# Performance work log

Measured on AMD Instinct MI355X. Metric: run time of the kernel, lower is better.

The kernel has to match this reference:

```python
import jax, jax.numpy as jnp
import numpy as np


def setup_inputs() -> dict:
    key = jax.random.key(0)
    k1, k2, k3, k4 = jax.random.split(key, 4)
    N, E, F, H = 100000, 1600000, 128, 128
    x = jax.random.normal(k1, (N, F), dtype=jnp.float32)
    edge_index = jax.random.randint(k2, (2, E), 0, N, dtype=jnp.int64)
    W1 = jax.random.normal(k3, (F, H), dtype=jnp.float32) * (1.0 / np.sqrt(F))
    b1 = jnp.zeros((H,), dtype=jnp.float32)
    W2 = jax.random.normal(k4, (H, H), dtype=jnp.float32) * (1.0 / np.sqrt(H))
    b2 = jnp.zeros((H,), dtype=jnp.float32)
    return {"x": x, "edge_index": edge_index, "W1": W1, "b1": b1, "W2": W2, "b2": b2}


def reference(x, edge_index, W1, b1, W2, b2):
    # Two-layer cached GCN: norm is computed once (cached) and reused by both layers.
    N = x.shape[0]
    loops = jnp.arange(N, dtype=edge_index.dtype)
    src = jnp.concatenate([edge_index[0], loops])  # add self-loops
    dst = jnp.concatenate([edge_index[1], loops])
    # symmetric GCN normalization: deg^-1/2[src] * deg^-1/2[dst]
    deg = jax.ops.segment_sum(jnp.ones_like(dst, dtype=x.dtype), dst, num_segments=N)
    dinv = jnp.where(deg > 0, jax.lax.rsqrt(deg), 0.0)
    norm = dinv[src] * dinv[dst]  # [E+N]

    def conv(h, W, b):
        h = h @ W  # dense transform before sparse aggregate (cheaper: out_dim small)
        msg = norm[:, None] * h[src]  # gather + scale
        return jax.ops.segment_sum(msg, dst, num_segments=N) + b

    h = jax.nn.relu(conv(x, W1, b1))
    # dropout is identity in eval mode (deterministic reference)
    return conv(h, W2, b2)
```

## Files before the change

### kernel.cpp

```cpp
#include <hip/hip_runtime.h>


#define BKT_SHIFT 7
#define BKT_NODES 128
#define CH 4096
#define MAXBKT 1024

typedef _Float16 half4v __attribute__((ext_vector_type(4)));
typedef _Float16 half8v __attribute__((ext_vector_type(8)));
typedef float float4v __attribute__((ext_vector_type(4)));

__global__ __launch_bounds__(256) void k_prep(const float* __restrict__ W1,
                                              const float* __restrict__ W2,
                                              _Float16* __restrict__ wt1,
                                              _Float16* __restrict__ wt2,
                                              int* __restrict__ bcnt,
                                              int* __restrict__ dcnt, int nbkt) {
    int i = blockIdx.x * 256 + threadIdx.x;
    if (i < 16384) {
        int k = i >> 7, c = i & 127;
        wt1[c * 128 + k] = (_Float16)W1[i];
    } else {
        int j = i - 16384;
        int k = j >> 7, c = j & 127;
        wt2[c * 128 + k] = (_Float16)W2[j];
    }
    if (i < nbkt) bcnt[i] = 0;
    if (i < 2) dcnt[i] = 0;
}

__global__ __launch_bounds__(256) void k_bincount_scan(const int* __restrict__ dst,
                                                       int* __restrict__ bcnt,
                                                       int* __restrict__ bofs,
                                                       int* __restrict__ bcur,
                                                       int* __restrict__ dcnt,
                                                       int E, int nbkt, int nblocks) {
    __shared__ int sh[MAXBKT];
    const int t = threadIdx.x;
    for (int i = t; i < nbkt; i += 256) sh[i] = 0;
    __syncthreads();
    for (long long e = (long long)blockIdx.x * 256 + t; e < E;
         e += (long long)nblocks * 256)
        atomicAdd(&sh[dst[e] >> BKT_SHIFT], 1);
    __syncthreads();
    for (int i = t; i < nbkt; i += 256)
        if (sh[i]) atomicAdd(&bcnt[i], sh[i]);
    __threadfence();
    __syncthreads();
    __shared__ int last;
    if (t == 0) last = (atomicAdd(&dcnt[0], 1) == nblocks - 1);
    __syncthreads();
    if (!last) return;
    __threadfence();
    int v[4];
    int s = 0;
    for (int k = 0; k < 4; k++) {
        int idx = t * 4 + k;
        v[k] = (idx < nbkt) ? atomicAdd(&bcnt[idx], 0) : 0;
        s += v[k];
    }
    __syncthreads();
    int x = s;
    sh[t] = x;
    __syncthreads();
    for (int o = 1; o < 256; o <<= 1) {
        int y = (t >= o) ? sh[t - o] : 0;
        __syncthreads();
        x += y;
        sh[t] = x;
        __syncthreads();
    }
    int run = x - s;
    for (int k = 0; k < 4; k++) {
        int idx = t * 4 + k;
        if (idx < nbkt) { bofs[idx] = run; bcur[idx] = run; }
        run += v[k];
    }
    if (t == 0) bofs[nbkt] = E;
}

__global__ __launch_bounds__(256) void k_binfill(const int* __restrict__ src,
                                                 const int* __restrict__ dst,
                                                 int* __restrict__ bcur,
                                                 unsigned* __restrict__ recs,
                                                 int E, int nbkt) {
    __shared__ unsigned stage[CH];
    __shared__ unsigned short stageb[CH];
    __shared__ int cnt[MAXBKT];
    __shared__ int base[MAXBKT];
    const int t = threadIdx.x;
    const long long c0 = (long long)blockIdx.x * CH;

    for (int i = t; i < nbkt; i += 256) cnt[i] = 0;
    __syncthreads();

    for (int k = 0; k < CH / 256; k++) {
        int i = k * 256 + t;
        long long e = c0 + i;
        if (e < E) {
            int d = dst[e];
            int b = d >> BKT_SHIFT;
            stage[i] = ((unsigned)(d & (BKT_NODES - 1)) << 17) | (unsigned)src[e];
            stageb[i] = (unsigned short)b;
            atomicAdd(&cnt[b], 1);
        }
    }
    __syncthreads();

    for (int i = t; i < nbkt; i += 256) {
        int c = cnt[i];
        base[i] = c ? atomicAdd(&bcur[i], c) : 0;
        cnt[i] = 0;
    }
    __syncthreads();

    for (int k = 0; k < CH / 256; k++) {
        int i = k * 256 + t;
        if (c0 + i < E) {
            int b = stageb[i];
            int p = base[b] + atomicAdd(&cnt[b], 1);
            recs[p] = stage[i];
        }
    }
}

__global__ __launch_bounds__(256) void k_deg_bins(const unsigned* __restrict__ recs,
                                                  const int* __restrict__ bofs,
                                                  int* __restrict__ deg, int n) {
    __shared__ int cnt[BKT_NODES];
    const int b = blockIdx.x, t = threadIdx.x;
    if (t < BKT_NODES) cnt[t] = 0;
    __syncthreads();
    const int beg = bofs[b], end = bofs[b + 1];
    for (int j = beg + t; j < end; j += 256)
        atomicAdd(&cnt[recs[j] >> 17], 1);
    __syncthreads();
    const int d0 = b << BKT_SHIFT;
    if (t < BKT_NODES && d0 + t < n) deg[d0 + t] = cnt[t];
}

__global__ __launch_bounds__(256) void k_scan12(const int* __restrict__ deg,
                                                float* __restrict__ dinv,
                                                int* __restrict__ ofs,
                                                int* __restrict__ sums,
                                                int* __restrict__ dcnt,
                                                int n, int nblocks) {
    __shared__ int sh[256];
    const int t = threadIdx.x;
    const int i = blockIdx.x * 256 + t;
    int v = (i < n) ? deg[i] : 0;
    if (i < n) dinv[i] = rsqrtf((float)v + 1.0f);
    int x = v;
    sh[t] = x;
    __syncthreads();
    for (int o = 1; o < 256; o <<= 1) {
        int y = (t >= o) ? sh[t - o] : 0;
        __syncthreads();
        x += y;
        sh[t] = x;
        __syncthreads();
    }
    if (i < n) ofs[i] = x - v;
    if (t == 255) atomicExch(&sums[blockIdx.x], x);
    __threadfence();
    __syncthreads();
    __shared__ int last;
    if (t == 0) last = (atomicAdd(&dcnt[1], 1) == nblocks - 1);
    __syncthreads();
    if (!last) return;
    __threadfence();
    int vv[4];
    int s = 0;
    for (int k = 0; k < 4; k++) {
        int idx = t * 4 + k;
        vv[k] = (idx < nblocks) ? atomicAdd(&sums[idx], 0) : 0;
        s += vv[k];
    }
    __syncthreads();
    int xx = s;
    sh[t] = xx;
    __syncthreads();
    for (int o = 1; o < 256; o <<= 1) {
        int y = (t >= o) ? sh[t - o] : 0;
        __syncthreads();
        xx += y;
        sh[t] = xx;
        __syncthreads();
    }
    int run = xx - s;
    for (int k = 0; k < 4; k++) {
        int idx = t * 4 + k;
        if (idx < nblocks) sums[idx] = run;
        run += vv[k];
    }
}

__global__ void k_scan3(int* __restrict__ ofs, const int* __restrict__ sums, int n, int E) {
    int i = blockIdx.x * 256 + threadIdx.x;
    if (i < n) ofs[i] += sums[blockIdx.x];
    if (i == 0) ofs[n] = E;
}

__global__ __launch_bounds__(256) void k_fill_bins(const unsigned* __restrict__ recs,
                                                   const int* __restrict__ bofs,
                                                   const int* __restrict__ ofs,
                                                   int* __restrict__ col, int n) {
    __shared__ int cur[BKT_NODES];
    const int b = blockIdx.x, t = threadIdx.x;
    const int d0 = b << BKT_SHIFT;
    if (t < BKT_NODES) cur[t] = (d0 + t < n) ? ofs[d0 + t] : 0;
    __syncthreads();
    const int beg = bofs[b], end = bofs[b + 1];
    for (int j = beg + t; j < end; j += 256) {
        unsigned r = recs[j];
        int p = atomicAdd(&cur[r >> 17], 1);
        col[p] = (int)(r & 0x1FFFF);
    }
}

__global__ __launch_bounds__(256, 4) void k_gemm_mfma(const float* __restrict__ in,
                                                      const _Float16* __restrict__ Wt,
                                                      const float* __restrict__ dinv,
                                                      _Float16* __restrict__ out, int n) {
    __shared__ _Float16 Bl[128][136];
    const int t = threadIdx.x;
    const int row0 = blockIdx.x * 64;

    for (int i = t; i < 128 * 16; i += 256) {
        int r = i >> 4, c8 = i & 15;
        *(half8v*)&Bl[r][c8 * 8] = *(const half8v*)&Wt[r * 128 + c8 * 8];
    }
    __syncthreads();

    const int wave = t >> 6;
    const int lane = t & 63;
    const int m0 = wave * 16;
    const int ml = lane & 15;
    const int quad = lane >> 4;

    int r = row0 + m0 + ml;
    if (r >= n) r = n - 1;

    float4v acc[8] = {};
#pragma unroll
    for (int kc = 0; kc < 4; kc++) {
        const float* ap = in + (size_t)r * 128 + kc * 32 + quad * 8;
        float4v v0 = *(const float4v*)ap;
        float4v v1 = *(const float4v*)(ap + 4);
        half8v a;
#pragma unroll
        for (int k = 0; k < 4; k++) {
            a[k] = (_Float16)v0[k];
            a[4 + k] = (_Float16)v1[k];
        }
#pragma unroll
        for (int nt = 0; nt < 8; nt++) {
            half8v b = *(const half8v*)&Bl[nt * 16 + ml][kc * 32 + quad * 8];
            acc[nt] = __builtin_amdgcn_mfma_f32_16x16x32_f16(a, b, acc[nt], 0, 0, 0);
        }
    }

    int nr = n - row0;
    if (nr > 64) nr = 64;
#pragma unroll
    for (int reg = 0; reg < 4; reg++) {
        int rr = m0 + quad * 4 + reg;
        if (rr < nr) {
            float dv = dinv[row0 + rr];
#pragma unroll
            for (int nt = 0; nt < 8; nt++)
                out[(size_t)(row0 + rr) * 128 + nt * 16 + ml] =
                    (_Float16)(acc[nt][reg] * dv);
        }
    }
}

__global__ __launch_bounds__(512, 4) void k_agg_gemm(const int* __restrict__ ofs,
                                                     const int* __restrict__ col,
                                                     const float* __restrict__ dinv,
                                                     const half4v* __restrict__ ts,
                                                     const float* __restrict__ bias,
                                                     const _Float16* __restrict__ Wt2,
                                                     _Float16* __restrict__ outt, int n) {
    __shared__ __align__(16) _Float16 hl[16][136];
    const int t = threadIdx.x;
    const int row0 = blockIdx.x * 16;
    const int r16 = t >> 5;
    const int lane = t & 31;
    const int row = row0 + r16;

    float4 acc = make_float4(0.f, 0.f, 0.f, 0.f);
    float dd = 0.f;
    if (row < n) {
        dd = dinv[row];
        int beg = ofs[row];
        int end = ofs[row + 1];
        half4v sv = ts[(size_t)row * 32 + lane];
        acc.x = (float)sv[0]; acc.y = (float)sv[1];
        acc.z = (float)sv[2]; acc.w = (float)sv[3];
        int j = beg;
        for (; j + 3 < end; j += 4) {
            int s0 = col[j], s1 = col[j + 1], s2 = col[j + 2], s3 = col[j + 3];
            half4v v0 = ts[(size_t)s0 * 32 + lane];
            half4v v1 = ts[(size_t)s1 * 32 + lane];
            half4v v2 = ts[(size_t)s2 * 32 + lane];
            half4v v3 = ts[(size_t)s3 * 32 + lane];
            acc.x += (float)v0[0] + (float)v1[0] + (float)v2[0] + (float)v3[0];
            acc.y += (float)v0[1] + (float)v1[1] + (float)v2[1] + (float)v3[1];
            acc.z += (float)v0[2] + (float)v1[2] + (float)v2[2] + (float)v3[2];
            acc.w += (float)v0[3] + (float)v1[3] + (float)v2[3] + (float)v3[3];
        }
        for (; j < end; j++) {
            half4v v = ts[(size_t)col[j] * 32 + lane];
            acc.x += (float)v[0];
            acc.y += (float)v[1];
            acc.z += (float)v[2];
            acc.w += (float)v[3];
        }
    }
    float4 bv = *(const float4*)&bias[lane * 4];
    half4v hv;
    hv[0] = (_Float16)fmaxf(bv.x + dd * acc.x, 0.f);
    hv[1] = (_Float16)fmaxf(bv.y + dd * acc.y, 0.f);
    hv[2] = (_Float16)fmaxf(bv.z + dd * acc.z, 0.f);
    hv[3] = (_Float16)fmaxf(bv.w + dd * acc.w, 0.f);
    *(half4v*)&hl[r16][lane * 4] = hv;
    __syncthreads();

    const int w = t >> 6;
    const int l = t & 63;
    const int ml = l & 15;
    const int quad = l >> 4;

    float4v acc2 = {};
#pragma unroll
    for (int kc = 0; kc < 4; kc++) {
        half8v a = *(const half8v*)&hl[ml][kc * 32 + quad * 8];
        half8v b = *(const half8v*)&Wt2[(size_t)(w * 16 + ml) * 128 + kc * 32 + quad * 8];
        acc2 = __builtin_amdgcn_mfma_f32_16x16x32_f16(a, b, acc2, 0, 0, 0);
    }
#pragma unroll
    for (int reg = 0; reg < 4; reg++) {
        int node = row0 + quad * 4 + reg;
        if (node < n) {
            float dv = dinv[node];
            outt[(size_t)node * 128 + w * 16 + ml] = (_Float16)(acc2[reg] * dv);
        }
    }
}

__global__ __launch_bounds__(256) void k_agg_csr32(const int* __restrict__ ofs,
                                                   const int* __restrict__ col,
                                                   const float* __restrict__ dinv,
                                                   const half4v* __restrict__ ts,
                                                   const float* __restrict__ bias,
                                                   float* __restrict__ out, int n) {
    int gid = blockIdx.x * 256 + threadIdx.x;
    int row = gid >> 5;
    int lane = gid & 31;
    if (row >= n) return;

    float dd = dinv[row];
    int beg = ofs[row];
    int end = ofs[row + 1];

    half4v sv = ts[(size_t)row * 32 + lane];
    float4 acc = make_float4((float)sv[0], (float)sv[1], (float)sv[2], (float)sv[3]);

    int j = beg;
    for (; j + 3 < end; j += 4) {
        int s0 = col[j], s1 = col[j + 1], s2 = col[j + 2], s3 = col[j + 3];
        half4v v0 = ts[(size_t)s0 * 32 + lane];
        half4v v1 = ts[(size_t)s1 * 32 + lane];
        half4v v2 = ts[(size_t)s2 * 32 + lane];
        half4v v3 = ts[(size_t)s3 * 32 + lane];
        acc.x += (float)v0[0] + (float)v1[0] + (float)v2[0] + (float)v3[0];
        acc.y += (float)v0[1] + (float)v1[1] + (float)v2[1] + (float)v3[1];
        acc.z += (float)v0[2] + (float)v1[2] + (float)v2[2] + (float)v3[2];
        acc.w += (float)v0[3] + (float)v1[3] + (float)v2[3] + (float)v3[3];
    }
    for (; j < end; j++) {
        half4v v = ts[(size_t)col[j] * 32 + lane];
        acc.x += (float)v[0];
        acc.y += (float)v[1];
        acc.z += (float)v[2];
        acc.w += (float)v[3];
    }

    float4 bv = *(const float4*)&bias[lane * 4];
    float4 o;
    o.x = bv.x + dd * acc.x;
    o.y = bv.y + dd * acc.y;
    o.z = bv.z + dd * acc.z;
    o.w = bv.w + dd * acc.w;
    *(float4*)&out[(size_t)row * 128 + lane * 4] = o;
}

extern "C" void kernel_launch(void* const* d_in, const int* in_sizes, int n_in,
                              void* d_out, int out_size, void* d_ws, size_t ws_size,
                              hipStream_t stream) {
    const int N = in_sizes[0] / 128;
    const int E = in_sizes[1] / 2;
    const float* x  = (const float*)d_in[0];
    const int*   ei = (const int*)d_in[1];
    const float* W1 = (const float*)d_in[2];
    const float* b1 = (const float*)d_in[3];
    const float* W2 = (const float*)d_in[4];
    const float* b2 = (const float*)d_in[5];

    const int* src = ei;
    const int* dst = ei + E;

    const int nb_n  = (N + 255) / 256;
    const int NBKT  = (N + BKT_NODES - 1) / BKT_NODES;

    _Float16* t    = (_Float16*)d_ws;
    _Float16* wt1  = t + (size_t)N * 128;
    _Float16* wt2  = wt1 + 16384;
    float*    dinv = (float*)(wt2 + 16384);
    int*      ofs  = (int*)(dinv + N);
    int*      deg  = ofs + N + 1;
    int*      sums = deg + N;
    unsigned* recs = (unsigned*)(sums + ((nb_n + 255) & ~255));
    int*      col  = (int*)(recs + E);
    int*      bofs = col + E;
    int*      bcur = bofs + NBKT + 1;
    int*      bcnt = bcur + NBKT;
    int*      dcnt = bcnt + NBKT;

    _Float16* ts1 = (_Float16*)d_out;
    float*    out = (float*)d_out;

    const int nb_g = (N + 63) / 64;
    const int nb_f = (N + 15) / 16;
    const int nb_a = (int)(((long long)N * 32 + 255) / 256);
    const int nb_c = (int)(((long long)E + CH - 1) / CH);

    k_prep<<<128, 256, 0, stream>>>(W1, W2, wt1, wt2, bcnt, dcnt, NBKT);
    k_bincount_scan<<<256, 256, 0, stream>>>(dst, bcnt, bofs, bcur, dcnt, E, NBKT, 256);
    k_binfill<<<nb_c, 256, 0, stream>>>(src, dst, bcur, recs, E, NBKT);
    k_deg_bins<<<NBKT, 256, 0, stream>>>(recs, bofs, deg, N);
    k_scan12<<<nb_n, 256, 0, stream>>>(deg, dinv, ofs, sums, dcnt, N, nb_n);
    k_scan3<<<nb_n, 256, 0, stream>>>(ofs, sums, N, E);
    k_fill_bins<<<NBKT, 256, 0, stream>>>(recs, bofs, ofs, col, N);

    k_gemm_mfma<<<nb_g, 256, 0, stream>>>(x, wt1, dinv, ts1, N);

    k_agg_gemm<<<nb_f, 512, 0, stream>>>(ofs, col, dinv, (const half4v*)ts1, b1, wt2, t, N);

    k_agg_csr32<<<nb_a, 256, 0, stream>>>(ofs, col, dinv, (const half4v*)t, b2, out, N);
}
```

Baseline: 372.0 us.

## Fuse degree, scan and CSR fill per bucket; split layer-2 agg and GEMM

Merges the per-bucket degree count, the global prefix scan and the column fill into one kernel. It does this by computing node offsets locally from bucket base offsets, which removes three launches and the deg/sums buffers. The fused aggregate+GEMM kernel for layer 1 is replaced by a plain CSR aggregate that writes fp16 ReLU output, followed by a templated MFMA GEMM that reads fp16 input. The binfill chunk size is doubled. The extra launch and the round trip of the hidden activations through memory trade against better occupancy in the aggregation.

New measurement: 328.1 us. 1.13x faster.

```diff
diff --git a/kernel.cpp b/kernel.cpp
--- a/kernel.cpp
+++ b/kernel.cpp
@@ -3,7 +3,7 @@
 
 #define BKT_SHIFT 7
 #define BKT_NODES 128
-#define CH 4096
+#define CH 8192
 #define MAXBKT 1024
 
 typedef _Float16 half4v __attribute__((ext_vector_type(4)));
@@ -124,101 +124,55 @@
     }
 }
 
-__global__ __launch_bounds__(256) void k_deg_bins(const unsigned* __restrict__ recs,
+__global__ __launch_bounds__(256) void k_fill_all(const unsigned* __restrict__ recs,
                                                   const int* __restrict__ bofs,
-                                                  int* __restrict__ deg, int n) {
+                                                  float* __restrict__ dinv,
+                                                  int* __restrict__ ofs,
+                                                  int* __restrict__ col,
+                                                  int n, int E) {
     __shared__ int cnt[BKT_NODES];
+    __shared__ int sc[BKT_NODES];
     const int b = blockIdx.x, t = threadIdx.x;
+    const int beg = bofs[b], end = bofs[b + 1];
+
     if (t < BKT_NODES) cnt[t] = 0;
     __syncthreads();
-    const int beg = bofs[b], end = bofs[b + 1];
     for (int j = beg + t; j < end; j += 256)
         atomicAdd(&cnt[recs[j] >> 17], 1);
     __syncthreads();
+
+    int v = 0, x = 0;
+    if (t < BKT_NODES) { v = cnt[t]; x = v; sc[t] = x; }
+    __syncthreads();
+    for (int o = 1; o < BKT_NODES; o <<= 1) {
+        int y = (t >= o && t < BKT_NODES) ? sc[t - o] : 0;
+        __syncthreads();
+        if (t < BKT_NODES) { x += y; sc[t] = x; }
+        __syncthreads();
+    }
+
     const int d0 = b << BKT_SHIFT;
-    if (t < BKT_NODES && d0 + t < n) deg[d0 + t] = cnt[t];
-}
-
-__global__ __launch_bounds__(256) void k_scan12(const int* __restrict__ deg,
-                                                float* __restrict__ dinv,
-                                                int* __restrict__ ofs,
-                                                int* __restrict__ sums,
-                                                int* __restrict__ dcnt,
-                                                int n, int nblocks) {
-    __shared__ int sh[256];
-    const int t = threadIdx.x;
-    const int i = blockIdx.x * 256 + t;
-    int v = (i < n) ? deg[i] : 0;
-    if (i < n) dinv[i] = rsqrtf((float)v + 1.0f);
-    int x = v;
-    sh[t] = x;
-    __syncthreads();
-    for (int o = 1; o < 256; o <<= 1) {
-        int y = (t >= o) ? sh[t - o] : 0;
-        __syncthreads();
-        x += y;
-        sh[t] = x;
-        __syncthreads();
-    }
-    if (i < n) ofs[i] = x - v;
-    if (t == 255) atomicExch(&sums[blockIdx.x], x);
-    __threadfence();
-    __syncthreads();
-    __shared__ int last;
-    if (t == 0) last = (atomicAdd(&dcnt[1], 1) == nblocks - 1);
-    __syncthreads();
-    if (!last) return;
-    __threadfence();
-    int vv[4];
-    int s = 0;
-    for (int k = 0; k < 4; k++) {
-        int idx = t * 4 + k;
-        vv[k] = (idx < nblocks) ? atomicAdd(&sums[idx], 0) : 0;
-        s += vv[k];
-    }
-    __syncthreads();
-    int xx = s;
-    sh[t] = xx;
-    __syncthreads();
-    for (int o = 1; o < 256; o <<= 1) {
-        int y = (t >= o) ? sh[t - o] : 0;
-        __syncthreads();
-        xx += y;
-        sh[t] = xx;
-        __syncthreads();
-    }
-    int run = xx - s;
-    for (int k = 0; k < 4; k++) {
-        int idx = t * 4 + k;
-        if (idx < nblocks) sums[idx] = run;
-        run += vv[k];
-    }
-}
-
-__global__ void k_scan3(int* __restrict__ ofs, const int* __restrict__ sums, int n, int E) {
-    int i = blockIdx.x * 256 + threadIdx.x;
-    if (i < n) ofs[i] += sums[blockIdx.x];
-    if (i == 0) ofs[n] = E;
-}
-
-__global__ __launch_bounds__(256) void k_fill_bins(const unsigned* __restrict__ recs,
-                                                   const int* __restrict__ bofs,
-                                                   const int* __restrict__ ofs,
-                                                   int* __restrict__ col, int n) {
-    __shared__ int cur[BKT_NODES];
-    const int b = blockIdx.x, t = threadIdx.x;
-    const int d0 = b << BKT_SHIFT;
-    if (t < BKT_NODES) cur[t] = (d0 + t < n) ? ofs[d0 + t] : 0;
-    __syncthreads();
-    const int beg = bofs[b], end = bofs[b + 1];
+    if (t < BKT_NODES) {
+        int off = beg + x - v;
+        int node = d0 + t;
+        if (node < n) {
+            ofs[node] = off;
+            dinv[node] = rsqrtf((float)v + 1.0f);
+        }
+        cnt[t] = off;
+    }
+    if (b == 0 && t == 0) ofs[n] = E;
+    __syncthreads();
+
     for (int j = beg + t; j < end; j += 256) {
         unsigned r = recs[j];
-        int p = atomicAdd(&cur[r >> 17], 1);
+        int p = atomicAdd(&cnt[r >> 17], 1);
         col[p] = (int)(r & 0x1FFFF);
     }
 }
 
-__global__ __launch_bounds__(256, 4) void k_gemm_mfma(const float* __restrict__ in,
+template <int IN_HALF>
+__global__ __launch_bounds__(256, 4) void k_gemm_mfma(const void* __restrict__ inp,
                                                       const _Float16* __restrict__ Wt,
                                                       const float* __restrict__ dinv,
                                                       _Float16* __restrict__ out, int n) {
@@ -244,19 +198,23 @@
     float4v acc[8] = {};
 #pragma unroll
     for (int kc = 0; kc < 4; kc++) {
-        const float* ap = in + (size_t)r * 128 + kc * 32 + quad * 8;
-        float4v v0 = *(const float4v*)ap;
-        float4v v1 = *(const float4v*)(ap + 4);
         half8v a;
-#pragma unroll
-        for (int k = 0; k < 4; k++) {
-            a[k] = (_Float16)v0[k];
-            a[4 + k] = (_Float16)v1[k];
+        if (IN_HALF) {
+            a = *(const half8v*)((const _Float16*)inp + (size_t)r * 128 + kc * 32 + quad * 8);
+        } else {
+            const float* ap = (const float*)inp + (size_t)r * 128 + kc * 32 + quad * 8;
+            float4v v0 = *(const float4v*)ap;
+            float4v v1 = *(const float4v*)(ap + 4);
+#pragma unroll
+            for (int k = 0; k < 4; k++) {
+                a[k] = (_Float16)v0[k];
+                a[4 + k] = (_Float16)v1[k];
+            }
         }
 #pragma unroll
         for (int nt = 0; nt < 8; nt++) {
-            half8v b = *(const half8v*)&Bl[nt * 16 + ml][kc * 32 + quad * 8];
-            acc[nt] = __builtin_amdgcn_mfma_f32_16x16x32_f16(a, b, acc[nt], 0, 0, 0);
+            half8v bfr = *(const half8v*)&Bl[nt * 16 + ml][kc * 32 + quad * 8];
+            acc[nt] = __builtin_amdgcn_mfma_f32_16x16x32_f16(a, bfr, acc[nt], 0, 0, 0);
         }
     }
 
@@ -275,86 +233,13 @@
     }
 }
 
-__global__ __launch_bounds__(512, 4) void k_agg_gemm(const int* __restrict__ ofs,
-                                                     const int* __restrict__ col,
-                                                     const float* __restrict__ dinv,
-                                                     const half4v* __restrict__ ts,
-                                                     const float* __restrict__ bias,
-                                                     const _Float16* __restrict__ Wt2,
-                                                     _Float16* __restrict__ outt, int n) {
-    __shared__ __align__(16) _Float16 hl[16][136];
-    const int t = threadIdx.x;
-    const int row0 = blockIdx.x * 16;
-    const int r16 = t >> 5;
-    const int lane = t & 31;
-    const int row = row0 + r16;
-
-    float4 acc = make_float4(0.f, 0.f, 0.f, 0.f);
-    float dd = 0.f;
-    if (row < n) {
-        dd = dinv[row];
-        int beg = ofs[row];
-        int end = ofs[row + 1];
-        half4v sv = ts[(size_t)row * 32 + lane];
-        acc.x = (float)sv[0]; acc.y = (float)sv[1];
-        acc.z = (float)sv[2]; acc.w = (float)sv[3];
-        int j = beg;
-        for (; j + 3 < end; j += 4) {
-            int s0 = col[j], s1 = col[j + 1], s2 = col[j + 2], s3 = col[j + 3];
-            half4v v0 = ts[(size_t)s0 * 32 + lane];
-            half4v v1 = ts[(size_t)s1 * 32 + lane];
-            half4v v2 = ts[(size_t)s2 * 32 + lane];
-            half4v v3 = ts[(size_t)s3 * 32 + lane];
-            acc.x += (float)v0[0] + (float)v1[0] + (float)v2[0] + (float)v3[0];
-            acc.y += (float)v0[1] + (float)v1[1] + (float)v2[1] + (float)v3[1];
-            acc.z += (float)v0[2] + (float)v1[2] + (float)v2[2] + (float)v3[2];
-            acc.w += (float)v0[3] + (float)v1[3] + (float)v2[3] + (float)v3[3];
-        }
-        for (; j < end; j++) {
-            half4v v = ts[(size_t)col[j] * 32 + lane];
-            acc.x += (float)v[0];
-            acc.y += (float)v[1];
-            acc.z += (float)v[2];
-            acc.w += (float)v[3];
-        }
-    }
-    float4 bv = *(const float4*)&bias[lane * 4];
-    half4v hv;
-    hv[0] = (_Float16)fmaxf(bv.x + dd * acc.x, 0.f);
-    hv[1] = (_Float16)fmaxf(bv.y + dd * acc.y, 0.f);
-    hv[2] = (_Float16)fmaxf(bv.z + dd * acc.z, 0.f);
-    hv[3] = (_Float16)fmaxf(bv.w + dd * acc.w, 0.f);
-    *(half4v*)&hl[r16][lane * 4] = hv;
-    __syncthreads();
-
-    const int w = t >> 6;
-    const int l = t & 63;
-    const int ml = l & 15;
-    const int quad = l >> 4;
-
-    float4v acc2 = {};
-#pragma unroll
-    for (int kc = 0; kc < 4; kc++) {
-        half8v a = *(const half8v*)&hl[ml][kc * 32 + quad * 8];
-        half8v b = *(const half8v*)&Wt2[(size_t)(w * 16 + ml) * 128 + kc * 32 + quad * 8];
-        acc2 = __builtin_amdgcn_mfma_f32_16x16x32_f16(a, b, acc2, 0, 0, 0);
-    }
-#pragma unroll
-    for (int reg = 0; reg < 4; reg++) {
-        int node = row0 + quad * 4 + reg;
-        if (node < n) {
-            float dv = dinv[node];
-            outt[(size_t)node * 128 + w * 16 + ml] = (_Float16)(acc2[reg] * dv);
-        }
-    }
-}
-
-__global__ __launch_bounds__(256) void k_agg_csr32(const int* __restrict__ ofs,
-                                                   const int* __restrict__ col,
-                                                   const float* __restrict__ dinv,
-                                                   const half4v* __restrict__ ts,
-                                                   const float* __restrict__ bias,
-                                                   float* __restrict__ out, int n) {
+template <int OUT_HALF>
+__global__ __launch_bounds__(256) void k_agg_csr(const int* __restrict__ ofs,
+                                                 const int* __restrict__ col,
+                                                 const float* __restrict__ dinv,
+                                                 const half4v* __restrict__ ts,
+                                                 const float* __restrict__ bias,
+                                                 void* __restrict__ outp, int n) {
     int gid = blockIdx.x * 256 + threadIdx.x;
     int row = gid >> 5;
     int lane = gid & 31;
@@ -388,12 +273,21 @@
     }
 
     float4 bv = *(const float4*)&bias[lane * 4];
-    float4 o;
-    o.x = bv.x + dd * acc.x;
-    o.y = bv.y + dd * acc.y;
-    o.z = bv.z + dd * acc.z;
-    o.w = bv.w + dd * acc.w;
-    *(float4*)&out[(size_t)row * 128 + lane * 4] = o;
+    if (OUT_HALF) {
+        half4v hv;
+        hv[0] = (_Float16)fmaxf(bv.x + dd * acc.x, 0.f);
+        hv[1] = (_Float16)fmaxf(bv.y + dd * acc.y, 0.f);
+        hv[2] = (_Float16)fmaxf(bv.z + dd * acc.z, 0.f);
+        hv[3] = (_Float16)fmaxf(bv.w + dd * acc.w, 0.f);
+        ((half4v*)outp)[(size_t)row * 32 + lane] = hv;
+    } else {
+        float4 o;
+        o.x = bv.x + dd * acc.x;
+        o.y = bv.y + dd * acc.y;
+        o.z = bv.z + dd * acc.z;
+        o.w = bv.w + dd * acc.w;
+        *(float4*)&((float*)outp)[(size_t)row * 128 + lane * 4] = o;
+    }
 }
 
 extern "C" void kernel_launch(void* const* d_in, const int* in_sizes, int n_in,
@@ -411,42 +305,35 @@
     const int* src = ei;
     const int* dst = ei + E;
 
-    const int nb_n  = (N + 255) / 256;
-    const int NBKT  = (N + BKT_NODES - 1) / BKT_NODES;
+    const int NBKT = (N + BKT_NODES - 1) / BKT_NODES;
 
     _Float16* t    = (_Float16*)d_ws;
     _Float16* wt1  = t + (size_t)N * 128;
     _Float16* wt2  = wt1 + 16384;
     float*    dinv = (float*)(wt2 + 16384);
     int*      ofs  = (int*)(dinv + N);
-    int*      deg  = ofs + N + 1;
-    int*      sums = deg + N;
-    unsigned* recs = (unsigned*)(sums + ((nb_n + 255) & ~255));
+    unsigned* recs = (unsigned*)(ofs + ((N + 2 + 255) & ~255));
     int*      col  = (int*)(recs + E);
     int*      bofs = col + E;
     int*      bcur = bofs + NBKT + 1;
     int*      bcnt = bcur + NBKT;
     int*      dcnt = bcnt + NBKT;
 
-    _Float16* ts1 = (_Float16*)d_out;
+    _Float16* h16 = (_Float16*)d_out;
     float*    out = (float*)d_out;
 
     const int nb_g = (N + 63) / 64;
-    const int nb_f = (N + 15) / 16;
     const int nb_a = (int)(((long long)N * 32 + 255) / 256);
     const int nb_c = (int)(((long long)E + CH - 1) / CH);
 
     k_prep<<<128, 256, 0, stream>>>(W1, W2, wt1, wt2, bcnt, dcnt, NBKT);
     k_bincount_scan<<<256, 256, 0, stream>>>(dst, bcnt, bofs, bcur, dcnt, E, NBKT, 256);
     k_binfill<<<nb_c, 256, 0, stream>>>(src, dst, bcur, recs, E, NBKT);
-    k_deg_bins<<<NBKT, 256, 0, stream>>>(recs, bofs, deg, N);
-    k_scan12<<<nb_n, 256, 0, stream>>>(deg, dinv, ofs, sums, dcnt, N, nb_n);
-    k_scan3<<<nb_n, 256, 0, stream>>>(ofs, sums, N, E);
-    k_fill_bins<<<NBKT, 256, 0, stream>>>(recs, bofs, ofs, col, N);
-
-    k_gemm_mfma<<<nb_g, 256, 0, stream>>>(x, wt1, dinv, ts1, N);
-
-    k_agg_gemm<<<nb_f, 512, 0, stream>>>(ofs, col, dinv, (const half4v*)ts1, b1, wt2, t, N);
-
-    k_agg_csr32<<<nb_a, 256, 0, stream>>>(ofs, col, dinv, (const half4v*)t, b2, out, N);
-}
+    k_fill_all<<<NBKT, 256, 0, stream>>>(recs, bofs, dinv, ofs, col, N, E);
+
+    k_gemm_mfma<0><<<nb_g, 256, 0, stream>>>(x, wt1, dinv, t, N);
+    k_agg_csr<1><<<nb_a, 256, 0, stream>>>(ofs, col, dinv, (const half4v*)t, b1, h16, N);
+
+    k_gemm_mfma<1><<<nb_g, 256, 0, stream>>>(h16, wt2, dinv, t, N);
+    k_agg_csr<0><<<nb_a, 256, 0, stream>>>(ofs, col, dinv, (const half4v*)t, b2, out, N);
+}
```
